# Kernel optimization log

Hardware: AMD Instinct MI355X
Metric: run time of the kernel (lower is better)

The kernel has to match this reference:

```python
import jax, jax.numpy as jnp
import numpy as np

EPS = 1e-5  # InstanceNorm2d default eps


def mesh_conv_point(x, neighbors, W, b):
    """MeshConvPoint: gather self+neighbor features, apply 1x(K+1) conv.
    x: [B, C, N]; neighbors: [B, N, K] int; W: [Cout, C, K+1]; b: [Cout]
    returns [B, Cout, N]
    """
    # gather neighbor features per batch: [B, C, N, K]
    g = jax.vmap(lambda xb, nb: xb[:, nb])(x, neighbors)
    G = jnp.concatenate([x[..., None], g], axis=-1)  # [B, C, N, K+1]
    return jnp.einsum('bcnk,ock->bon', G, W) + b[None, :, None]


def instance_norm(x):
    # InstanceNorm2d (affine=False) on [B, C, N, 1] == normalize over N per (b,c)
    mu = jnp.mean(x, axis=2, keepdims=True)
    var = jnp.var(x, axis=2, keepdims=True)
    return (x - mu) * jax.lax.rsqrt(var + EPS)


def setup_inputs() -> dict:
    key = jax.random.key(0)
    ks = jax.random.split(key, 10)
    B, Cin, Cout, N, K = 2, 256, 128, 30000, 6
    from_up = jax.random.normal(ks[0], (B, Cin, N), dtype=jnp.float32)
    from_down = jax.random.normal(ks[1], (B, Cout, N), dtype=jnp.float32)
    neighbors = jax.random.randint(ks[2], (B, N, K), 0, N)
    s = 0.05
    W_up = jax.random.normal(ks[3], (Cout, Cin, K + 1), dtype=jnp.float32) * s
    b_up = jnp.zeros((Cout,), dtype=jnp.float32)
    W_1 = jax.random.normal(ks[4], (Cout, 2 * Cout, K + 1), dtype=jnp.float32) * s
    b_1 = jnp.zeros((Cout,), dtype=jnp.float32)
    W_2 = jax.random.normal(ks[5], (Cout, Cout, K + 1), dtype=jnp.float32) * s
    b_2 = jnp.zeros((Cout,), dtype=jnp.float32)
    return {"from_up": from_up, "from_down": from_down, "neighbors": neighbors,
            "W_up": W_up, "b_up": b_up, "W_1": W_1, "b_1": b_1,
            "W_2": W_2, "b_2": b_2}


def reference(from_up, from_down, neighbors, W_up, b_up, W_1, b_1, W_2, b_2):
    # up_conv + squeeze(3)
    x1 = mesh_conv_point(from_up, neighbors, W_up, b_up)          # [B, Cout, N]
    # transfer_data: concat skip features along channels
    x1 = jnp.concatenate([x1, from_down], axis=1)                 # [B, 2*Cout, N]
    x1 = mesh_conv_point(x1, neighbors, W_1, b_1)                 # [B, Cout, N]
    x1 = instance_norm(x1)                                        # bn[0]
    # one conv2 block (blocks=1): conv + instance norm + residual
    x2 = mesh_conv_point(x1, neighbors, W_2, b_2)
    x2 = instance_norm(x2)                                        # bn[1]
    x2 = x2 + x1                                                  # residual
    return x2                                                     # [B, Cout, N]
```

## Files before the change

kernel.cpp:

```cpp
#include <hip/hip_runtime.h>

typedef __attribute__((ext_vector_type(8))) short short8;
typedef __attribute__((ext_vector_type(4))) float f32x4;

static __device__ __forceinline__ float bf2f(unsigned short u) {
    unsigned int x = ((unsigned int)u) << 16;
    union { unsigned int i; float f; } c; c.i = x; return c.f;
}
static __device__ __forceinline__ unsigned short f2bf(float f) {
    union { float f; unsigned int i; } c; c.f = f;
    unsigned int x = c.i;
    unsigned int r = (x + 0x7FFFu + ((x >> 16) & 1u)) >> 16;
    return (unsigned short)r;
}
static __device__ __forceinline__ void glds16(const char* g, char* l) {
    __builtin_amdgcn_global_load_lds(
        (const __attribute__((address_space(1))) unsigned int*)g,
        (__attribute__((address_space(3))) unsigned int*)l, 16, 0, 0);
}

__global__ void prepack_w(const float* __restrict__ W, unsigned short* __restrict__ Wp,
                          int Cin, int S) {
    int tid = blockIdx.x * blockDim.x + threadIdx.x;
    if (tid >= S * 512) return;
    int lane = tid & 63;
    int f = (tid >> 6) & 7;
    int s = tid >> 9;
    int o = f * 16 + (lane & 15);
    int kbase = s * 32 + 8 * (lane >> 4);
    unsigned short* dst = Wp + (size_t)tid * 8;
#pragma unroll
    for (int j = 0; j < 8; ++j) {
        int kk = kbase + j;
        int t = kk / Cin;
        int c = kk - t * Cin;
        dst[j] = f2bf(W[((size_t)o * Cin + c) * 7 + t]);
    }
}

__global__ void prepack_w_scaled(const float* __restrict__ W, const float2* __restrict__ stats,
                                 unsigned short* __restrict__ Wp, int Cin, int S) {
    int tid = blockIdx.x * blockDim.x + threadIdx.x;
    if (tid >= 2 * S * 512) return;
    int b = tid / (S * 512);
    int rem = tid - b * S * 512;
    int lane = rem & 63;
    int f = (rem >> 6) & 7;
    int s = rem >> 9;
    int o = f * 16 + (lane & 15);
    int kbase = s * 32 + 8 * (lane >> 4);
    unsigned short* dst = Wp + (size_t)tid * 8;
#pragma unroll
    for (int j = 0; j < 8; ++j) {
        int kk = kbase + j;
        int t = kk / Cin;
        int c = kk - t * Cin;
        float scale = stats[b * 128 + c].y;
        dst[j] = f2bf(W[((size_t)o * Cin + c) * 7 + t] * scale);
    }
}

__global__ void fold_bias2(const float* __restrict__ W2, const float* __restrict__ b2,
                           const float2* __restrict__ stats, float* __restrict__ b2out) {
    int b = blockIdx.x, o = threadIdx.x;
    float sum = 0.f;
    for (int c = 0; c < 128; ++c) {
        float2 st = stats[b * 128 + c];
        float sm = st.x * st.y;
        float ws = 0.f;
#pragma unroll
        for (int t = 0; t < 7; ++t) ws += W2[((size_t)o * 128 + c) * 7 + t];
        sum += ws * sm;
    }
    b2out[b * 128 + o] = b2[o] - sum;
}

__global__ void transpose_cast(const float* __restrict__ in, unsigned short* __restrict__ out,
                               int C, int N, int ldo, int coff) {
    __shared__ float tile[32][33];
    int b = blockIdx.z;
    int n0 = blockIdx.x * 32;
    int c0 = blockIdx.y * 32;
    const float* inb = in + (size_t)b * C * N;
    unsigned short* outb = out + (size_t)b * N * ldo;
    int tx = threadIdx.x, ty = threadIdx.y;
#pragma unroll
    for (int i = 0; i < 32; i += 8) {
        int c = c0 + ty + i, n = n0 + tx;
        float v = 0.f;
        if (n < N) v = inb[(size_t)c * N + n];
        tile[ty + i][tx] = v;
    }
    __syncthreads();
#pragma unroll
    for (int i = 0; i < 32; i += 8) {
        int n = n0 + ty + i, c = c0 + tx;
        if (n < N) outb[(size_t)n * ldo + coff + c] = f2bf(tile[tx][ty + i]);
    }
}

template<int CS, int LD, bool STATS>
__global__ __launch_bounds__(256, 2) void conv_gemm(
    const unsigned short* __restrict__ src,
    const int* __restrict__ nbrs,
    const unsigned short* __restrict__ Wp, size_t w_bstride_bytes,
    const float* __restrict__ bias, int bias_bstride,
    unsigned short* __restrict__ dst,
    float2* __restrict__ part,
    int N, int coff)
{
    constexpr int ROWB = CS * 2;
    constexpr int SPT  = CS / 32;
    constexpr int S    = SPT * 7;

    const int tid  = threadIdx.x;
    const int lane = tid & 63;
    const int wid  = tid >> 6;
    const int pg   = wid & 1;
    const int h    = wid >> 1;
    const int l15  = lane & 15;
    const int ks   = lane >> 4;
    const int b    = blockIdx.y;
    const int pblk = blockIdx.x * 128;

    const char* srcb = (const char*)src + (size_t)b * N * ROWB;
    const char* wbc  = (const char*)Wp + (size_t)b * w_bstride_bytes;

    __shared__ char smem[4 * 8192 + 4 * 8192];

    int roffA[28];
    if (wid < 2) {
        int p = pblk + wid * 64 + lane;
        int pe = p < N ? p : N - 1;
        int offs[7];
        offs[0] = pe * ROWB;
        const int* nb = nbrs + ((size_t)b * N + pe) * 6;
#pragma unroll
        for (int t = 1; t < 7; ++t) offs[t] = nb[t - 1] * ROWB;
#pragma unroll
        for (int t = 0; t < 7; ++t)
#pragma unroll
            for (int i = 0; i < 4; ++i)
                roffA[t * 4 + i] = __shfl(offs[t], i * 16 + (lane >> 2));
    }
    asm volatile("s_waitcnt vmcnt(0)" ::: "memory");
    __builtin_amdgcn_sched_barrier(0);

    const int asw = (((lane & 3) ^ ((lane >> 2) & 3) ^ ((lane >> 4) & 3)) << 4);

    auto stage_all = [&](int t, int kk, int s, int buf) {
        if (wid < 2) {
#pragma unroll
            for (int i = 0; i < 4; ++i)
                glds16(srcb + roffA[t * 4 + i] + kk * 64 + asw,
                       smem + buf * 8192 + wid * 4096 + i * 1024);
        } else {
            const char* gw = wbc + (size_t)s * 8192 + (wid - 2) * 4096 + lane * 16;
            char* lw = smem + 32768 + buf * 8192 + (wid - 2) * 4096;
#pragma unroll
            for (int i = 0; i < 4; ++i)
                glds16(gw + i * 1024, lw + i * 1024);
        }
    };

    f32x4 acc[4][4];
#pragma unroll
    for (int rg = 0; rg < 4; ++rg)
#pragma unroll
        for (int fi = 0; fi < 4; ++fi) acc[rg][fi] = (f32x4){0.f, 0.f, 0.f, 0.f};

    stage_all(0, 0, 0, 0);
    stage_all(1 / SPT, 1 % SPT, 1, 1);

    const int arsw = (((l15 & 3) ^ ((l15 >> 2) & 3)) << 4);

#pragma unroll
    for (int t = 0; t < 7; ++t) {
#pragma unroll
        for (int kk = 0; kk < SPT; ++kk) {
            const int s = t * SPT + kk;
            if (s + 2 < S) {
                const int s2 = s + 2;
                stage_all(s2 / SPT, s2 % SPT, s2, s2 & 3);
            }
            if (s + 2 < S)      { asm volatile("s_waitcnt vmcnt(8)" ::: "memory"); }
            else if (s + 1 < S) { asm volatile("s_waitcnt vmcnt(4)" ::: "memory"); }
            else                { asm volatile("s_waitcnt vmcnt(0)" ::: "memory"); }
            __builtin_amdgcn_sched_barrier(0);
            __builtin_amdgcn_s_barrier();
            __builtin_amdgcn_sched_barrier(0);

            const char* Ab = smem + (s & 3) * 8192;
            const char* Wb = smem + 32768 + (s & 3) * 8192;
            short8 a[4], w[4];
#pragma unroll
            for (int rg = 0; rg < 4; ++rg)
                a[rg] = *(const short8*)(Ab + (pg * 64 + rg * 16 + l15) * 64 +
                                         ((ks << 4) ^ arsw));
#pragma unroll
            for (int fi = 0; fi < 4; ++fi)
                w[fi] = *(const short8*)(Wb + (h * 4 + fi) * 1024 + lane * 16);
            __builtin_amdgcn_s_setprio(1);
#pragma unroll
            for (int rg = 0; rg < 4; ++rg)
#pragma unroll
                for (int fi = 0; fi < 4; ++fi)
                    acc[rg][fi] = __builtin_amdgcn_mfma_f32_16x16x32_bf16(
                        a[rg], w[fi], acc[rg][fi], 0, 0, 0);
            __builtin_amdgcn_s_setprio(0);
        }
    }

    const float* biasb = bias + (size_t)b * bias_bstride + h * 64;
    float bias_v[4];
#pragma unroll
    for (int fi = 0; fi < 4; ++fi) bias_v[fi] = biasb[fi * 16 + l15];

    unsigned short* dstb = dst + (size_t)b * N * LD + coff + h * 64;
#pragma unroll
    for (int rg = 0; rg < 4; ++rg) {
#pragma unroll
        for (int r = 0; r < 4; ++r) {
            int p = pblk + pg * 64 + rg * 16 + ks * 4 + r;
            if (p < N) {
#pragma unroll
                for (int fi = 0; fi < 4; ++fi)
                    dstb[(size_t)p * LD + fi * 16 + l15] = f2bf(acc[rg][fi][r] + bias_v[fi]);
            }
        }
    }

    if constexpr (STATS) {
        float s4[4], q4[4];
#pragma unroll
        for (int fi = 0; fi < 4; ++fi) { s4[fi] = 0.f; q4[fi] = 0.f; }
#pragma unroll
        for (int rg = 0; rg < 4; ++rg) {
#pragma unroll
            for (int r = 0; r < 4; ++r) {
                int p = pblk + pg * 64 + rg * 16 + ks * 4 + r;
                if (p < N) {
#pragma unroll
                    for (int fi = 0; fi < 4; ++fi) {
                        float v = acc[rg][fi][r] + bias_v[fi];
                        s4[fi] += v; q4[fi] += v * v;
                    }
                }
            }
        }
#pragma unroll
        for (int fi = 0; fi < 4; ++fi) {
            s4[fi] += __shfl_xor(s4[fi], 16); s4[fi] += __shfl_xor(s4[fi], 32);
            q4[fi] += __shfl_xor(q4[fi], 16); q4[fi] += __shfl_xor(q4[fi], 32);
        }
        __syncthreads();
        float* shs = (float*)smem;
        float* shq = shs + 256;
        if (lane < 16) {
#pragma unroll
            for (int fi = 0; fi < 4; ++fi) {
                shs[wid * 64 + fi * 16 + l15] = s4[fi];
                shq[wid * 64 + fi * 16 + l15] = q4[fi];
            }
        }
        __syncthreads();
        if (tid < 128) {
            int c = tid;
            int hh = c >> 6, cl = c & 63;
            float ss = shs[(2 * hh) * 64 + cl] + shs[(2 * hh + 1) * 64 + cl];
            float qq = shq[(2 * hh) * 64 + cl] + shq[(2 * hh + 1) * 64 + cl];
            part[((size_t)b * gridDim.x + blockIdx.x) * 128 + c] = make_float2(ss, qq);
        }
    }
}

__global__ void stats_final(const float2* __restrict__ part, float2* __restrict__ stats,
                            int N, int NB) {
    int b = blockIdx.x;
    int c = threadIdx.x & 127;
    int r = threadIdx.x >> 7;
    float s = 0.f, sq = 0.f;
    const float2* p = part + (size_t)b * NB * 128 + c;
#pragma unroll 4
    for (int i = r; i < NB; i += 8) {
        float2 v = p[(size_t)i * 128];
        s += v.x; sq += v.y;
    }
    __shared__ float shs[8][128], shq[8][128];
    shs[r][c] = s; shq[r][c] = sq;
    __syncthreads();
    if (r == 0) {
#pragma unroll
        for (int i = 1; i < 8; ++i) { s += shs[i][c]; sq += shq[i][c]; }
        float mu = s / N;
        float var = sq / N - mu * mu;
        stats[b * 128 + c] = make_float2(mu, rsqrtf(var + 1e-5f));
    }
}

__global__ void final_k(const unsigned short* __restrict__ z, const unsigned short* __restrict__ x1,
                        const float2* __restrict__ stats1, const float2* __restrict__ stats2,
                        float* __restrict__ out, int N) {
    __shared__ float tile[32][33];
    int b = blockIdx.z;
    int n0 = blockIdx.x * 32, o0 = blockIdx.y * 32;
    int tx = threadIdx.x, ty = threadIdx.y;
    const unsigned short* zb = z  + (size_t)b * N * 128;
    const unsigned short* xb = x1 + (size_t)b * N * 128;
    float2 st1 = stats1[b * 128 + o0 + tx];
    float2 st2 = stats2[b * 128 + o0 + tx];
#pragma unroll
    for (int i = 0; i < 32; i += 8) {
        int n = n0 + ty + i;
        float v = 0.f;
        if (n < N) {
            float zv = bf2f(zb[(size_t)n * 128 + o0 + tx]);
            float xv = bf2f(xb[(size_t)n * 128 + o0 + tx]);
            v = (zv - st2.x) * st2.y + (xv - st1.x) * st1.y;
        }
        tile[ty + i][tx] = v;
    }
    __syncthreads();
    float* ob = out + (size_t)b * 128 * N;
#pragma unroll
    for (int i = 0; i < 32; i += 8) {
        int o = o0 + ty + i, n = n0 + tx;
        if (n < N) ob[(size_t)o * N + n] = tile[tx][ty + i];
    }
}

extern "C" void kernel_launch(void* const* d_in, const int* in_sizes, int n_in,
                              void* d_out, int out_size, void* d_ws, size_t ws_size,
                              hipStream_t stream) {
    const float* from_up   = (const float*)d_in[0];
    const float* from_down = (const float*)d_in[1];
    const int*   neighbors = (const int*)d_in[2];
    const float* W_up = (const float*)d_in[3];
    const float* b_up = (const float*)d_in[4];
    const float* W_1  = (const float*)d_in[5];
    const float* b_1  = (const float*)d_in[6];
    const float* W_2  = (const float*)d_in[7];
    const float* b_2  = (const float*)d_in[8];
    float* out = (float*)d_out;

    const int B = 2, N = 30000;
    const int S1 = 56, S3 = 28;
    const int NBLK = (N + 127) / 128;

    char* ws = (char*)d_ws;
    size_t off = 0;
    auto alloc = [&](size_t bytes) {
        char* p = ws + off;
        off += (bytes + 255) & ~(size_t)255;
        return p;
    };
    unsigned short* upT   = (unsigned short*)alloc((size_t)B * N * 256 * 2);
    unsigned short* catT  = (unsigned short*)alloc((size_t)B * N * 256 * 2);
    unsigned short* x1    = (unsigned short*)alloc((size_t)B * N * 128 * 2);
    unsigned short* Wp0   = (unsigned short*)alloc((size_t)S1 * 512 * 8 * 2);
    unsigned short* Wp1   = (unsigned short*)alloc((size_t)S1 * 512 * 8 * 2);
    unsigned short* Wp2b  = (unsigned short*)alloc((size_t)B * S3 * 512 * 8 * 2);
    float*  b2fold = (float*)alloc((size_t)B * 128 * 4);
    float2* part   = (float2*)alloc((size_t)B * NBLK * 128 * 8);
    float2* stats1 = (float2*)alloc((size_t)B * 128 * 8);
    float2* stats2 = (float2*)alloc((size_t)B * 128 * 8);
    unsigned short* zbuf = upT;

    prepack_w<<<(S1 * 512 + 255) / 256, 256, 0, stream>>>(W_up, Wp0, 256, S1);
    prepack_w<<<(S1 * 512 + 255) / 256, 256, 0, stream>>>(W_1,  Wp1, 256, S1);

    dim3 tb(32, 8);
    transpose_cast<<<dim3((N + 31) / 32, 256 / 32, B), tb, 0, stream>>>(from_up, upT, 256, N, 256, 0);
    transpose_cast<<<dim3((N + 31) / 32, 128 / 32, B), tb, 0, stream>>>(from_down, catT, 128, N, 256, 128);

    dim3 cgrid(NBLK, B);
    conv_gemm<256, 256, false><<<cgrid, 256, 0, stream>>>(
        upT, neighbors, Wp0, 0, b_up, 0, catT, nullptr, N, 0);
    conv_gemm<256, 128, true><<<cgrid, 256, 0, stream>>>(
        catT, neighbors, Wp1, 0, b_1, 0, x1, part, N, 0);
    stats_final<<<B, 1024, 0, stream>>>((const float2*)part, stats1, N, NBLK);

    prepack_w_scaled<<<(B * S3 * 512 + 255) / 256, 256, 0, stream>>>(W_2, stats1, Wp2b, 128, S3);
    fold_bias2<<<B, 128, 0, stream>>>(W_2, b_2, stats1, b2fold);

    conv_gemm<128, 128, true><<<cgrid, 256, 0, stream>>>(
        x1, neighbors, Wp2b, (size_t)S3 * 8192, b2fold, 128, zbuf, part, N, 0);
    stats_final<<<B, 1024, 0, stream>>>((const float2*)part, stats2, N, NBLK);

    final_k<<<dim3((N + 31) / 32, 4, B), tb, 0, stream>>>(zbuf, x1, stats1, stats2, out, N);
}
```

Before: 188.4 us.

## Double conv GEMM block tile to 256 points with 8 waves and deeper prefetch

The conv GEMM block grows from 128 to 256 points and from 4 to 8 waves. Every wave now shares the gather and weight staging work, where before two waves did each job. The weight tile in LDS is reused across twice as many points, and the pipeline issues its prefetch three stages ahead, after the barrier. The cost is fewer blocks (about 118 per batch), a larger LDS footprint (96KB) that may limit occupancy, and a reworked stats reduction across four point groups.

```diff
diff --git a/kernel.cpp b/kernel.cpp
--- a/kernel.cpp
+++ b/kernel.cpp
@@ -100,7 +100,7 @@
 }
 
 template<int CS, int LD, bool STATS>
-__global__ __launch_bounds__(256, 2) void conv_gemm(
+__global__ __launch_bounds__(512, 2) void conv_gemm(
     const unsigned short* __restrict__ src,
     const int* __restrict__ nbrs,
     const unsigned short* __restrict__ Wp, size_t w_bstride_bytes,
@@ -112,25 +112,26 @@
     constexpr int ROWB = CS * 2;
     constexpr int SPT  = CS / 32;
     constexpr int S    = SPT * 7;
+    constexpr int BUFB = 24576;
 
     const int tid  = threadIdx.x;
     const int lane = tid & 63;
     const int wid  = tid >> 6;
-    const int pg   = wid & 1;
-    const int h    = wid >> 1;
+    const int pg   = wid & 3;
+    const int h    = wid >> 2;
     const int l15  = lane & 15;
     const int ks   = lane >> 4;
     const int b    = blockIdx.y;
-    const int pblk = blockIdx.x * 128;
+    const int pblk = blockIdx.x * 256;
 
     const char* srcb = (const char*)src + (size_t)b * N * ROWB;
     const char* wbc  = (const char*)Wp + (size_t)b * w_bstride_bytes;
 
-    __shared__ char smem[4 * 8192 + 4 * 8192];
-
-    int roffA[28];
-    if (wid < 2) {
-        int p = pblk + wid * 64 + lane;
+    __shared__ char smem[4 * BUFB];
+
+    int roffA[14];
+    {
+        int p = pblk + wid * 32 + (lane & 31);
         int pe = p < N ? p : N - 1;
         int offs[7];
         offs[0] = pe * ROWB;
@@ -140,8 +141,8 @@
 #pragma unroll
         for (int t = 0; t < 7; ++t)
 #pragma unroll
-            for (int i = 0; i < 4; ++i)
-                roffA[t * 4 + i] = __shfl(offs[t], i * 16 + (lane >> 2));
+            for (int i = 0; i < 2; ++i)
+                roffA[t * 2 + i] = __shfl(offs[t], i * 16 + (lane >> 2));
     }
     asm volatile("s_waitcnt vmcnt(0)" ::: "memory");
     __builtin_amdgcn_sched_barrier(0);
@@ -149,18 +150,13 @@
     const int asw = (((lane & 3) ^ ((lane >> 2) & 3) ^ ((lane >> 4) & 3)) << 4);
 
     auto stage_all = [&](int t, int kk, int s, int buf) {
-        if (wid < 2) {
-#pragma unroll
-            for (int i = 0; i < 4; ++i)
-                glds16(srcb + roffA[t * 4 + i] + kk * 64 + asw,
-                       smem + buf * 8192 + wid * 4096 + i * 1024);
-        } else {
-            const char* gw = wbc + (size_t)s * 8192 + (wid - 2) * 4096 + lane * 16;
-            char* lw = smem + 32768 + buf * 8192 + (wid - 2) * 4096;
-#pragma unroll
-            for (int i = 0; i < 4; ++i)
-                glds16(gw + i * 1024, lw + i * 1024);
-        }
+        char* base = smem + buf * BUFB;
+#pragma unroll
+        for (int i = 0; i < 2; ++i)
+            glds16(srcb + roffA[t * 2 + i] + kk * 64 + asw,
+                   base + (wid * 2 + i) * 1024);
+        glds16(wbc + (size_t)s * 8192 + wid * 1024 + lane * 16,
+               base + 16384 + wid * 1024);
     };
 
     f32x4 acc[4][4];
@@ -171,6 +167,7 @@
 
     stage_all(0, 0, 0, 0);
     stage_all(1 / SPT, 1 % SPT, 1, 1);
+    stage_all(2 / SPT, 2 % SPT, 2, 2);
 
     const int arsw = (((l15 & 3) ^ ((l15 >> 2) & 3)) << 4);
 
@@ -179,19 +176,19 @@
 #pragma unroll
         for (int kk = 0; kk < SPT; ++kk) {
             const int s = t * SPT + kk;
-            if (s + 2 < S) {
-                const int s2 = s + 2;
-                stage_all(s2 / SPT, s2 % SPT, s2, s2 & 3);
-            }
-            if (s + 2 < S)      { asm volatile("s_waitcnt vmcnt(8)" ::: "memory"); }
-            else if (s + 1 < S) { asm volatile("s_waitcnt vmcnt(4)" ::: "memory"); }
+            if (s + 2 < S)      { asm volatile("s_waitcnt vmcnt(6)" ::: "memory"); }
+            else if (s + 1 < S) { asm volatile("s_waitcnt vmcnt(3)" ::: "memory"); }
             else                { asm volatile("s_waitcnt vmcnt(0)" ::: "memory"); }
             __builtin_amdgcn_sched_barrier(0);
             __builtin_amdgcn_s_barrier();
             __builtin_amdgcn_sched_barrier(0);
-
-            const char* Ab = smem + (s & 3) * 8192;
-            const char* Wb = smem + 32768 + (s & 3) * 8192;
+            if (s + 3 < S) {
+                const int s3 = s + 3;
+                stage_all(s3 / SPT, s3 % SPT, s3, s3 & 3);
+            }
+
+            const char* Ab = smem + (s & 3) * BUFB;
+            const char* Wb = Ab + 16384;
             short8 a[4], w[4];
 #pragma unroll
             for (int rg = 0; rg < 4; ++rg)
@@ -255,7 +252,7 @@
         }
         __syncthreads();
         float* shs = (float*)smem;
-        float* shq = shs + 256;
+        float* shq = shs + 512;
         if (lane < 16) {
 #pragma unroll
             for (int fi = 0; fi < 4; ++fi) {
@@ -267,8 +264,12 @@
         if (tid < 128) {
             int c = tid;
             int hh = c >> 6, cl = c & 63;
-            float ss = shs[(2 * hh) * 64 + cl] + shs[(2 * hh + 1) * 64 + cl];
-            float qq = shq[(2 * hh) * 64 + cl] + shq[(2 * hh + 1) * 64 + cl];
+            float ss = 0.f, qq = 0.f;
+#pragma unroll
+            for (int p4 = 0; p4 < 4; ++p4) {
+                ss += shs[(hh * 4 + p4) * 64 + cl];
+                qq += shq[(hh * 4 + p4) * 64 + cl];
+            }
             part[((size_t)b * gridDim.x + blockIdx.x) * 128 + c] = make_float2(ss, qq);
         }
     }
@@ -345,7 +346,7 @@
 
     const int B = 2, N = 30000;
     const int S1 = 56, S3 = 28;
-    const int NBLK = (N + 127) / 128;
+    const int NBLK = (N + 255) / 256;
 
     char* ws = (char*)d_ws;
     size_t off = 0;
@@ -374,16 +375,16 @@
     transpose_cast<<<dim3((N + 31) / 32, 128 / 32, B), tb, 0, stream>>>(from_down, catT, 128, N, 256, 128);
 
     dim3 cgrid(NBLK, B);
-    conv_gemm<256, 256, false><<<cgrid, 256, 0, stream>>>(
+    conv_gemm<256, 256, false><<<cgrid, 512, 0, stream>>>(
         upT, neighbors, Wp0, 0, b_up, 0, catT, nullptr, N, 0);
-    conv_gemm<256, 128, true><<<cgrid, 256, 0, stream>>>(
+    conv_gemm<256, 128, true><<<cgrid, 512, 0, stream>>>(
         catT, neighbors, Wp1, 0, b_1, 0, x1, part, N, 0);
     stats_final<<<B, 1024, 0, stream>>>((const float2*)part, stats1, N, NBLK);
 
     prepack_w_scaled<<<(B * S3 * 512 + 255) / 256, 256, 0, stream>>>(W_2, stats1, Wp2b, 128, S3);
     fold_bias2<<<B, 128, 0, stream>>>(W_2, b_2, stats1, b2fold);
 
-    conv_gemm<128, 128, true><<<cgrid, 256, 0, stream>>>(
+    conv_gemm<128, 128, true><<<cgrid, 512, 0, stream>>>(
         x1, neighbors, Wp2b, (size_t)S3 * 8192, b2fold, 128, zbuf, part, N, 0);
     stats_final<<<B, 1024, 0, stream>>>((const float2*)part, stats2, N, NBLK);
 
```

New measurement: 182.6 us. 3.1% less time.

## Load weights straight to registers and spread A gather across all waves

Applied to the files above, without the earlier changes.

Weight fragments are now loaded from global memory directly into registers, triple-buffered two steps ahead, instead of being staged through LDS. All four waves now share the gathered A-tile loads (two per wave) instead of only two waves issuing them, with a deeper three-step LDS prefetch. The goal is to cut LDS traffic and footprint and to balance load issue across waves. The cost is more register pressure from the three weight buffers and a modulo-3 buffer select that may not resolve at compile time unless the loop is fully unrolled.

```diff
diff --git a/kernel.cpp b/kernel.cpp
--- a/kernel.cpp
+++ b/kernel.cpp
@@ -126,11 +126,11 @@
     const char* srcb = (const char*)src + (size_t)b * N * ROWB;
     const char* wbc  = (const char*)Wp + (size_t)b * w_bstride_bytes;
 
-    __shared__ char smem[4 * 8192 + 4 * 8192];
-
-    int roffA[28];
-    if (wid < 2) {
-        int p = pblk + wid * 64 + lane;
+    __shared__ char smem[4 * 8192];
+
+    int roffA[14];
+    {
+        int p = pblk + wid * 32 + (lane & 31);
         int pe = p < N ? p : N - 1;
         int offs[7];
         offs[0] = pe * ROWB;
@@ -140,28 +140,27 @@
 #pragma unroll
         for (int t = 0; t < 7; ++t)
 #pragma unroll
-            for (int i = 0; i < 4; ++i)
-                roffA[t * 4 + i] = __shfl(offs[t], i * 16 + (lane >> 2));
+            for (int i = 0; i < 2; ++i)
+                roffA[t * 2 + i] = __shfl(offs[t], i * 16 + (lane >> 2));
     }
     asm volatile("s_waitcnt vmcnt(0)" ::: "memory");
     __builtin_amdgcn_sched_barrier(0);
 
     const int asw = (((lane & 3) ^ ((lane >> 2) & 3) ^ ((lane >> 4) & 3)) << 4);
 
-    auto stage_all = [&](int t, int kk, int s, int buf) {
-        if (wid < 2) {
-#pragma unroll
-            for (int i = 0; i < 4; ++i)
-                glds16(srcb + roffA[t * 4 + i] + kk * 64 + asw,
-                       smem + buf * 8192 + wid * 4096 + i * 1024);
-        } else {
-            const char* gw = wbc + (size_t)s * 8192 + (wid - 2) * 4096 + lane * 16;
-            char* lw = smem + 32768 + buf * 8192 + (wid - 2) * 4096;
-#pragma unroll
-            for (int i = 0; i < 4; ++i)
-                glds16(gw + i * 1024, lw + i * 1024);
-        }
+    auto stageA = [&](int sidx, int buf) {
+        int t = sidx / SPT, kk = sidx % SPT;
+        char* base = smem + buf * 8192;
+#pragma unroll
+        for (int i = 0; i < 2; ++i)
+            glds16(srcb + roffA[t * 2 + i] + kk * 64 + asw,
+                   base + (wid * 2 + i) * 1024);
     };
+    auto loadW = [&](int sidx, short8 w[4]) {
+        const short8* gw = (const short8*)(wbc + (size_t)sidx * 8192 + h * 4096) + lane;
+#pragma unroll
+        for (int fi = 0; fi < 4; ++fi) w[fi] = gw[fi * 64];
+    };
 
     f32x4 acc[4][4];
 #pragma unroll
@@ -169,46 +168,41 @@
 #pragma unroll
         for (int fi = 0; fi < 4; ++fi) acc[rg][fi] = (f32x4){0.f, 0.f, 0.f, 0.f};
 
-    stage_all(0, 0, 0, 0);
-    stage_all(1 / SPT, 1 % SPT, 1, 1);
+    short8 w0[4], w1[4], w2[4];
+    stageA(0, 0);
+    stageA(1, 1);
+    loadW(0, w0);
+    stageA(2, 2);
+    loadW(1, w1);
 
     const int arsw = (((l15 & 3) ^ ((l15 >> 2) & 3)) << 4);
 
 #pragma unroll
-    for (int t = 0; t < 7; ++t) {
-#pragma unroll
-        for (int kk = 0; kk < SPT; ++kk) {
-            const int s = t * SPT + kk;
-            if (s + 2 < S) {
-                const int s2 = s + 2;
-                stage_all(s2 / SPT, s2 % SPT, s2, s2 & 3);
-            }
-            if (s + 2 < S)      { asm volatile("s_waitcnt vmcnt(8)" ::: "memory"); }
-            else if (s + 1 < S) { asm volatile("s_waitcnt vmcnt(4)" ::: "memory"); }
-            else                { asm volatile("s_waitcnt vmcnt(0)" ::: "memory"); }
-            __builtin_amdgcn_sched_barrier(0);
-            __builtin_amdgcn_s_barrier();
-            __builtin_amdgcn_sched_barrier(0);
-
-            const char* Ab = smem + (s & 3) * 8192;
-            const char* Wb = smem + 32768 + (s & 3) * 8192;
-            short8 a[4], w[4];
-#pragma unroll
-            for (int rg = 0; rg < 4; ++rg)
-                a[rg] = *(const short8*)(Ab + (pg * 64 + rg * 16 + l15) * 64 +
-                                         ((ks << 4) ^ arsw));
+    for (int s = 0; s < S; ++s) {
+        if (s + 2 < S)      { asm volatile("s_waitcnt vmcnt(6)" ::: "memory"); }
+        else if (s + 1 < S) { asm volatile("s_waitcnt vmcnt(4)" ::: "memory"); }
+        else                { asm volatile("s_waitcnt vmcnt(0)" ::: "memory"); }
+        __builtin_amdgcn_sched_barrier(0);
+        __builtin_amdgcn_s_barrier();
+        __builtin_amdgcn_sched_barrier(0);
+        if (s + 3 < S) stageA(s + 3, (s + 3) & 3);
+        if (s + 2 < S) loadW(s + 2, (s % 3 == 0) ? w2 : (s % 3 == 1) ? w0 : w1);
+
+        const short8* w = (s % 3 == 0) ? w0 : (s % 3 == 1) ? w1 : w2;
+        const char* Ab = smem + (s & 3) * 8192;
+        short8 a[4];
+#pragma unroll
+        for (int rg = 0; rg < 4; ++rg)
+            a[rg] = *(const short8*)(Ab + (pg * 64 + rg * 16 + l15) * 64 +
+                                     ((ks << 4) ^ arsw));
+        __builtin_amdgcn_s_setprio(1);
+#pragma unroll
+        for (int rg = 0; rg < 4; ++rg)
 #pragma unroll
             for (int fi = 0; fi < 4; ++fi)
-                w[fi] = *(const short8*)(Wb + (h * 4 + fi) * 1024 + lane * 16);
-            __builtin_amdgcn_s_setprio(1);
-#pragma unroll
-            for (int rg = 0; rg < 4; ++rg)
-#pragma unroll
-                for (int fi = 0; fi < 4; ++fi)
-                    acc[rg][fi] = __builtin_amdgcn_mfma_f32_16x16x32_bf16(
-                        a[rg], w[fi], acc[rg][fi], 0, 0, 0);
-            __builtin_amdgcn_s_setprio(0);
-        }
+                acc[rg][fi] = __builtin_amdgcn_mfma_f32_16x16x32_bf16(
+                    a[rg], w[fi], acc[rg][fi], 0, 0, 0);
+        __builtin_amdgcn_s_setprio(0);
     }
 
     const float* biasb = bias + (size_t)b * bias_bstride + h * 64;
```

New measurement: 196.3 us. 1.04x slower.

## Restructure conv GEMM to two waves each computing full 128 outputs, merge small kernels

Applied to the files above, without the earlier changes.

The conv GEMM drops from four waves (two loading gathered rows, two loading weights, each computing a 64x64 quadrant) to two waves. Each wave now loads both A and W and computes 64 points by 128 outputs, with triple-buffered shared memory and the stage issued after the barrier. This doubles the accumulators per wave to raise MFMA work per load and cut redundant A fragment reads. Separately, the prepack, transpose and bias-fold launches are merged to reduce kernel launch count. In exchange, register pressure rises and there are fewer waves per CU to hide gather latency.

```diff
diff --git a/kernel.cpp b/kernel.cpp
--- a/kernel.cpp
+++ b/kernel.cpp
@@ -19,16 +19,21 @@
         (__attribute__((address_space(3))) unsigned int*)l, 16, 0, 0);
 }
 
-__global__ void prepack_w(const float* __restrict__ W, unsigned short* __restrict__ Wp,
-                          int Cin, int S) {
+__global__ void prepack_w2(const float* __restrict__ Wa, const float* __restrict__ Wb,
+                           unsigned short* __restrict__ Wpa, unsigned short* __restrict__ Wpb,
+                           int S) {
     int tid = blockIdx.x * blockDim.x + threadIdx.x;
-    if (tid >= S * 512) return;
-    int lane = tid & 63;
-    int f = (tid >> 6) & 7;
-    int s = tid >> 9;
+    if (tid >= 2 * S * 512) return;
+    const float* W = (tid < S * 512) ? Wa : Wb;
+    unsigned short* Wp = (tid < S * 512) ? Wpa : Wpb;
+    int rem = (tid < S * 512) ? tid : tid - S * 512;
+    const int Cin = 256;
+    int lane = rem & 63;
+    int f = (rem >> 6) & 7;
+    int s = rem >> 9;
     int o = f * 16 + (lane & 15);
     int kbase = s * 32 + 8 * (lane >> 4);
-    unsigned short* dst = Wp + (size_t)tid * 8;
+    unsigned short* dst = Wp + (size_t)rem * 8;
 #pragma unroll
     for (int j = 0; j < 8; ++j) {
         int kk = kbase + j;
@@ -38,51 +43,56 @@
     }
 }
 
-__global__ void prepack_w_scaled(const float* __restrict__ W, const float2* __restrict__ stats,
-                                 unsigned short* __restrict__ Wp, int Cin, int S) {
-    int tid = blockIdx.x * blockDim.x + threadIdx.x;
-    if (tid >= 2 * S * 512) return;
-    int b = tid / (S * 512);
-    int rem = tid - b * S * 512;
-    int lane = rem & 63;
-    int f = (rem >> 6) & 7;
-    int s = rem >> 9;
-    int o = f * 16 + (lane & 15);
-    int kbase = s * 32 + 8 * (lane >> 4);
-    unsigned short* dst = Wp + (size_t)tid * 8;
-#pragma unroll
-    for (int j = 0; j < 8; ++j) {
-        int kk = kbase + j;
-        int t = kk / Cin;
-        int c = kk - t * Cin;
-        float scale = stats[b * 128 + c].y;
-        dst[j] = f2bf(W[((size_t)o * Cin + c) * 7 + t] * scale);
-    }
-}
-
-__global__ void fold_bias2(const float* __restrict__ W2, const float* __restrict__ b2,
-                           const float2* __restrict__ stats, float* __restrict__ b2out) {
-    int b = blockIdx.x, o = threadIdx.x;
-    float sum = 0.f;
-    for (int c = 0; c < 128; ++c) {
-        float2 st = stats[b * 128 + c];
-        float sm = st.x * st.y;
-        float ws = 0.f;
-#pragma unroll
-        for (int t = 0; t < 7; ++t) ws += W2[((size_t)o * 128 + c) * 7 + t];
-        sum += ws * sm;
-    }
-    b2out[b * 128 + o] = b2[o] - sum;
-}
-
-__global__ void transpose_cast(const float* __restrict__ in, unsigned short* __restrict__ out,
-                               int C, int N, int ldo, int coff) {
+__global__ void prepack_scaled_fold(const float* __restrict__ W, const float2* __restrict__ stats,
+                                    unsigned short* __restrict__ Wp, const float* __restrict__ b2,
+                                    float* __restrict__ b2out, int S, int nPre) {
+    if ((int)blockIdx.x < nPre) {
+        int tid = blockIdx.x * 256 + threadIdx.x;
+        const int Cin = 128;
+        int b = tid / (S * 512);
+        int rem = tid - b * S * 512;
+        int lane = rem & 63;
+        int f = (rem >> 6) & 7;
+        int s = rem >> 9;
+        int o = f * 16 + (lane & 15);
+        int kbase = s * 32 + 8 * (lane >> 4);
+        unsigned short* dst = Wp + (size_t)tid * 8;
+#pragma unroll
+        for (int j = 0; j < 8; ++j) {
+            int kk = kbase + j;
+            int t = kk / Cin;
+            int c = kk - t * Cin;
+            float scale = stats[b * 128 + c].y;
+            dst[j] = f2bf(W[((size_t)o * Cin + c) * 7 + t] * scale);
+        }
+    } else {
+        int b = threadIdx.x >> 7, o = threadIdx.x & 127;
+        float sum = 0.f;
+        for (int c = 0; c < 128; ++c) {
+            float2 st = stats[b * 128 + c];
+            float sm = st.x * st.y;
+            float ws = 0.f;
+#pragma unroll
+            for (int t = 0; t < 7; ++t) ws += W[((size_t)o * 128 + c) * 7 + t];
+            sum += ws * sm;
+        }
+        b2out[b * 128 + o] = b2[o] - sum;
+    }
+}
+
+__global__ void transpose_cast2(const float* __restrict__ up, const float* __restrict__ down,
+                                unsigned short* __restrict__ upT, unsigned short* __restrict__ catT,
+                                int N) {
     __shared__ float tile[32][33];
     int b = blockIdx.z;
+    int y = blockIdx.y;
+    const float* in;  unsigned short* outp;  int c0, coff;
+    if (y < 8) { in = up;   outp = upT;  c0 = y * 32;       coff = 0;   }
+    else       { in = down; outp = catT; c0 = (y - 8) * 32; coff = 128; }
+    int C = (y < 8) ? 256 : 128;
     int n0 = blockIdx.x * 32;
-    int c0 = blockIdx.y * 32;
     const float* inb = in + (size_t)b * C * N;
-    unsigned short* outb = out + (size_t)b * N * ldo;
+    unsigned short* outb = outp + (size_t)b * N * 256;
     int tx = threadIdx.x, ty = threadIdx.y;
 #pragma unroll
     for (int i = 0; i < 32; i += 8) {
@@ -95,12 +105,12 @@
 #pragma unroll
     for (int i = 0; i < 32; i += 8) {
         int n = n0 + ty + i, c = c0 + tx;
-        if (n < N) outb[(size_t)n * ldo + coff + c] = f2bf(tile[tx][ty + i]);
+        if (n < N) outb[(size_t)n * 256 + coff + c] = f2bf(tile[tx][ty + i]);
     }
 }
 
 template<int CS, int LD, bool STATS>
-__global__ __launch_bounds__(256, 2) void conv_gemm(
+__global__ __launch_bounds__(128, 2) void conv_gemm(
     const unsigned short* __restrict__ src,
     const int* __restrict__ nbrs,
     const unsigned short* __restrict__ Wp, size_t w_bstride_bytes,
@@ -115,9 +125,7 @@
 
     const int tid  = threadIdx.x;
     const int lane = tid & 63;
-    const int wid  = tid >> 6;
-    const int pg   = wid & 1;
-    const int h    = wid >> 1;
+    const int wv   = tid >> 6;
     const int l15  = lane & 15;
     const int ks   = lane >> 4;
     const int b    = blockIdx.y;
@@ -126,11 +134,11 @@
     const char* srcb = (const char*)src + (size_t)b * N * ROWB;
     const char* wbc  = (const char*)Wp + (size_t)b * w_bstride_bytes;
 
-    __shared__ char smem[4 * 8192 + 4 * 8192];
+    __shared__ char smem[3 * 16384];
 
     int roffA[28];
-    if (wid < 2) {
-        int p = pblk + wid * 64 + lane;
+    {
+        int p = pblk + wv * 64 + lane;
         int pe = p < N ? p : N - 1;
         int offs[7];
         offs[0] = pe * ROWB;
@@ -148,100 +156,90 @@
 
     const int asw = (((lane & 3) ^ ((lane >> 2) & 3) ^ ((lane >> 4) & 3)) << 4);
 
-    auto stage_all = [&](int t, int kk, int s, int buf) {
-        if (wid < 2) {
-#pragma unroll
-            for (int i = 0; i < 4; ++i)
-                glds16(srcb + roffA[t * 4 + i] + kk * 64 + asw,
-                       smem + buf * 8192 + wid * 4096 + i * 1024);
-        } else {
-            const char* gw = wbc + (size_t)s * 8192 + (wid - 2) * 4096 + lane * 16;
-            char* lw = smem + 32768 + buf * 8192 + (wid - 2) * 4096;
-#pragma unroll
-            for (int i = 0; i < 4; ++i)
-                glds16(gw + i * 1024, lw + i * 1024);
-        }
+    auto stage = [&](int sidx, int buf) {
+        int t = sidx / SPT, kk = sidx - t * SPT;
+        char* base = smem + buf * 16384;
+#pragma unroll
+        for (int i = 0; i < 4; ++i)
+            glds16(srcb + roffA[t * 4 + i] + kk * 64 + asw,
+                   base + wv * 4096 + i * 1024);
+        const char* gw = wbc + (size_t)sidx * 8192 + wv * 4096 + lane * 16;
+        char* lw = base + 8192 + wv * 4096;
+#pragma unroll
+        for (int j = 0; j < 4; ++j)
+            glds16(gw + j * 1024, lw + j * 1024);
     };
 
-    f32x4 acc[4][4];
+    f32x4 acc[4][8];
 #pragma unroll
     for (int rg = 0; rg < 4; ++rg)
 #pragma unroll
-        for (int fi = 0; fi < 4; ++fi) acc[rg][fi] = (f32x4){0.f, 0.f, 0.f, 0.f};
-
-    stage_all(0, 0, 0, 0);
-    stage_all(1 / SPT, 1 % SPT, 1, 1);
+        for (int fi = 0; fi < 8; ++fi) acc[rg][fi] = (f32x4){0.f, 0.f, 0.f, 0.f};
+
+    stage(0, 0);
+    stage(1, 1);
 
     const int arsw = (((l15 & 3) ^ ((l15 >> 2) & 3)) << 4);
 
 #pragma unroll
-    for (int t = 0; t < 7; ++t) {
-#pragma unroll
-        for (int kk = 0; kk < SPT; ++kk) {
-            const int s = t * SPT + kk;
-            if (s + 2 < S) {
-                const int s2 = s + 2;
-                stage_all(s2 / SPT, s2 % SPT, s2, s2 & 3);
-            }
-            if (s + 2 < S)      { asm volatile("s_waitcnt vmcnt(8)" ::: "memory"); }
-            else if (s + 1 < S) { asm volatile("s_waitcnt vmcnt(4)" ::: "memory"); }
-            else                { asm volatile("s_waitcnt vmcnt(0)" ::: "memory"); }
-            __builtin_amdgcn_sched_barrier(0);
-            __builtin_amdgcn_s_barrier();
-            __builtin_amdgcn_sched_barrier(0);
-
-            const char* Ab = smem + (s & 3) * 8192;
-            const char* Wb = smem + 32768 + (s & 3) * 8192;
-            short8 a[4], w[4];
-#pragma unroll
-            for (int rg = 0; rg < 4; ++rg)
-                a[rg] = *(const short8*)(Ab + (pg * 64 + rg * 16 + l15) * 64 +
-                                         ((ks << 4) ^ arsw));
-#pragma unroll
-            for (int fi = 0; fi < 4; ++fi)
-                w[fi] = *(const short8*)(Wb + (h * 4 + fi) * 1024 + lane * 16);
-            __builtin_amdgcn_s_setprio(1);
-#pragma unroll
-            for (int rg = 0; rg < 4; ++rg)
-#pragma unroll
-                for (int fi = 0; fi < 4; ++fi)
-                    acc[rg][fi] = __builtin_amdgcn_mfma_f32_16x16x32_bf16(
-                        a[rg], w[fi], acc[rg][fi], 0, 0, 0);
-            __builtin_amdgcn_s_setprio(0);
-        }
-    }
-
-    const float* biasb = bias + (size_t)b * bias_bstride + h * 64;
-    float bias_v[4];
-#pragma unroll
-    for (int fi = 0; fi < 4; ++fi) bias_v[fi] = biasb[fi * 16 + l15];
-
-    unsigned short* dstb = dst + (size_t)b * N * LD + coff + h * 64;
+    for (int s = 0; s < S; ++s) {
+        if (s + 1 < S) { asm volatile("s_waitcnt vmcnt(8)" ::: "memory"); }
+        else           { asm volatile("s_waitcnt vmcnt(0)" ::: "memory"); }
+        __builtin_amdgcn_sched_barrier(0);
+        __builtin_amdgcn_s_barrier();
+        __builtin_amdgcn_sched_barrier(0);
+        if (s + 2 < S) stage(s + 2, (s + 2) % 3);
+
+        const char* base = smem + (s % 3) * 16384;
+        short8 a[4], w[8];
+#pragma unroll
+        for (int rg = 0; rg < 4; ++rg)
+            a[rg] = *(const short8*)(base + wv * 4096 + (rg * 16 + l15) * 64 +
+                                     ((ks << 4) ^ arsw));
+#pragma unroll
+        for (int fi = 0; fi < 8; ++fi)
+            w[fi] = *(const short8*)(base + 8192 + fi * 1024 + lane * 16);
+        __builtin_amdgcn_s_setprio(1);
+#pragma unroll
+        for (int rg = 0; rg < 4; ++rg)
+#pragma unroll
+            for (int fi = 0; fi < 8; ++fi)
+                acc[rg][fi] = __builtin_amdgcn_mfma_f32_16x16x32_bf16(
+                    a[rg], w[fi], acc[rg][fi], 0, 0, 0);
+        __builtin_amdgcn_s_setprio(0);
+    }
+
+    const float* biasb = bias + (size_t)b * bias_bstride;
+    float bias_v[8];
+#pragma unroll
+    for (int fi = 0; fi < 8; ++fi) bias_v[fi] = biasb[fi * 16 + l15];
+
+    unsigned short* dstb = dst + (size_t)b * N * LD + coff;
 #pragma unroll
     for (int rg = 0; rg < 4; ++rg) {
 #pragma unroll
         for (int r = 0; r < 4; ++r) {
-            int p = pblk + pg * 64 + rg * 16 + ks * 4 + r;
+            int p = pblk + wv * 64 + rg * 16 + ks * 4 + r;
             if (p < N) {
 #pragma unroll
-                for (int fi = 0; fi < 4; ++fi)
+                for (int fi = 0; fi < 8; ++fi)
                     dstb[(size_t)p * LD + fi * 16 + l15] = f2bf(acc[rg][fi][r] + bias_v[fi]);
             }
         }
     }
 
     if constexpr (STATS) {
-        float s4[4], q4[4];
-#pragma unroll
-        for (int fi = 0; fi < 4; ++fi) { s4[fi] = 0.f; q4[fi] = 0.f; }
+        float s4[8], q4[8];
+#pragma unroll
+        for (int fi = 0; fi < 8; ++fi) { s4[fi] = 0.f; q4[fi] = 0.f; }
 #pragma unroll
         for (int rg = 0; rg < 4; ++rg) {
 #pragma unroll
             for (int r = 0; r < 4; ++r) {
-                int p = pblk + pg * 64 + rg * 16 + ks * 4 + r;
+                int p = pblk + wv * 64 + rg * 16 + ks * 4 + r;
                 if (p < N) {
 #pragma unroll
-                    for (int fi = 0; fi < 4; ++fi) {
+                    for (int fi = 0; fi < 8; ++fi) {
                         float v = acc[rg][fi][r] + bias_v[fi];
                         s4[fi] += v; q4[fi] += v * v;
                     }
@@ -249,7 +247,7 @@
             }
         }
 #pragma unroll
-        for (int fi = 0; fi < 4; ++fi) {
+        for (int fi = 0; fi < 8; ++fi) {
             s4[fi] += __shfl_xor(s4[fi], 16); s4[fi] += __shfl_xor(s4[fi], 32);
             q4[fi] += __shfl_xor(q4[fi], 16); q4[fi] += __shfl_xor(q4[fi], 32);
         }
@@ -258,17 +256,16 @@
         float* shq = shs + 256;
         if (lane < 16) {
 #pragma unroll
-            for (int fi = 0; fi < 4; ++fi) {
-                shs[wid * 64 + fi * 16 + l15] = s4[fi];
-                shq[wid * 64 + fi * 16 + l15] = q4[fi];
+            for (int fi = 0; fi < 8; ++fi) {
+                shs[wv * 128 + fi * 16 + l15] = s4[fi];
+                shq[wv * 128 + fi * 16 + l15] = q4[fi];
             }
         }
         __syncthreads();
-        if (tid < 128) {
+        {
             int c = tid;
-            int hh = c >> 6, cl = c & 63;
-            float ss = shs[(2 * hh) * 64 + cl] + shs[(2 * hh + 1) * 64 + cl];
-            float qq = shq[(2 * hh) * 64 + cl] + shq[(2 * hh + 1) * 64 + cl];
+            float ss = shs[c] + shs[128 + c];
+            float qq = shq[c] + shq[128 + c];
             part[((size_t)b * gridDim.x + blockIdx.x) * 128 + c] = make_float2(ss, qq);
         }
     }
@@ -366,24 +363,22 @@
     float2* stats2 = (float2*)alloc((size_t)B * 128 * 8);
     unsigned short* zbuf = upT;
 
-    prepack_w<<<(S1 * 512 + 255) / 256, 256, 0, stream>>>(W_up, Wp0, 256, S1);
-    prepack_w<<<(S1 * 512 + 255) / 256, 256, 0, stream>>>(W_1,  Wp1, 256, S1);
+    prepack_w2<<<(2 * S1 * 512 + 255) / 256, 256, 0, stream>>>(W_up, W_1, Wp0, Wp1, S1);
 
     dim3 tb(32, 8);
-    transpose_cast<<<dim3((N + 31) / 32, 256 / 32, B), tb, 0, stream>>>(from_up, upT, 256, N, 256, 0);
-    transpose_cast<<<dim3((N + 31) / 32, 128 / 32, B), tb, 0, stream>>>(from_down, catT, 128, N, 256, 128);
+    transpose_cast2<<<dim3((N + 31) / 32, 12, B), tb, 0, stream>>>(from_up, from_down, upT, catT, N);
 
     dim3 cgrid(NBLK, B);
-    conv_gemm<256, 256, false><<<cgrid, 256, 0, stream>>>(
+    conv_gemm<256, 256, false><<<cgrid, 128, 0, stream>>>(
         upT, neighbors, Wp0, 0, b_up, 0, catT, nullptr, N, 0);
-    conv_gemm<256, 128, true><<<cgrid, 256, 0, stream>>>(
+    conv_gemm<256, 128, true><<<cgrid, 128, 0, stream>>>(
         catT, neighbors, Wp1, 0, b_1, 0, x1, part, N, 0);
     stats_final<<<B, 1024, 0, stream>>>((const float2*)part, stats1, N, NBLK);
 
-    prepack_w_scaled<<<(B * S3 * 512 + 255) / 256, 256, 0, stream>>>(W_2, stats1, Wp2b, 128, S3);
-    fold_bias2<<<B, 128, 0, stream>>>(W_2, b_2, stats1, b2fold);
-
-    conv_gemm<128, 128, true><<<cgrid, 256, 0, stream>>>(
+    int nPre = (B * S3 * 512) / 256;
+    prepack_scaled_fold<<<nPre + 1, 256, 0, stream>>>(W_2, stats1, Wp2b, b_2, b2fold, S3, nPre);
+
+    conv_gemm<128, 128, true><<<cgrid, 128, 0, stream>>>(
         x1, neighbors, Wp2b, (size_t)S3 * 8192, b2fold, 128, zbuf, part, N, 0);
     stats_final<<<B, 1024, 0, stream>>>((const float2*)part, stats2, N, NBLK);
 
```

Result: slower. 199.3 us (+5.8%).
